# Performance work log

Measured on AMD Instinct MI355X. Metric: run time of the kernel, lower is better.

The kernel has to match this reference:

```python
import jax, jax.numpy as jnp
import numpy as np


def exp_segsum(x):
    """exp(segsum(x)) with the -inf mask folded into a zero mask (same math).
    x: (..., T) -> (..., T, T) lower-triangular decay matrix."""
    T = x.shape[-1]
    xr = jnp.broadcast_to(x[..., None], (*x.shape, T))  # (..., d, e) = x[..., d]
    lower = jnp.tril(jnp.ones((T, T), dtype=bool), -1)
    seg = jnp.cumsum(jnp.where(lower, xr, 0.0), axis=-2)
    incl = jnp.tril(jnp.ones((T, T), dtype=bool), 0)
    return jnp.where(incl, jnp.exp(seg), 0.0)


def ssd(x, A, B, C, chunk_size):
    """Mamba2 chunked structured state-space duality.
    x: (b, L, h, p); A: (b, L, h); B, C: (b, L, n) (shared across heads).
    Returns y: (b, L, h, p) and final state (b, h, p, n)."""
    b_, L_, H, P = x.shape
    c = L_ // chunk_size
    xm = x.reshape(b_, c, chunk_size, H, P)                      # b c l h p
    Am = A.reshape(b_, c, chunk_size, H).transpose(0, 3, 1, 2)   # b h c l
    Bm = B.reshape(b_, c, chunk_size, -1)                        # b c l n
    Cm = C.reshape(b_, c, chunk_size, -1)                        # b c l n
    A_cumsum = jnp.cumsum(Am, axis=-1)                           # b h c l
    Lmat = exp_segsum(Am)                                        # b h c l l
    # intra-chunk (diagonal block) outputs
    Y_diag = jnp.einsum('bcln,bcsn,bhcls,bcshp->bclhp', Cm, Bm, Lmat, xm)
    # per-chunk states
    decay_states = jnp.exp(A_cumsum[:, :, :, -1:] - A_cumsum)    # b h c l
    states = jnp.einsum('bcln,bhcl,bclhp->bchpn', Bm, decay_states, xm)
    init = jnp.zeros_like(states[:, :1])
    states = jnp.concatenate([init, states], axis=1)             # b (c+1) h p n
    # inter-chunk recurrence via segsum over chunk-level decays
    decay_chunk = exp_segsum(jnp.pad(A_cumsum[:, :, :, -1], ((0, 0), (0, 0), (1, 0))))
    new_states = jnp.einsum('bhzc,bchpn->bzhpn', decay_chunk, states)
    states, final_state = new_states[:, :-1], new_states[:, -1]
    # state -> output conversion
    decay_out = jnp.exp(A_cumsum)                                # b h c l
    Y_off = jnp.einsum('bcln,bchpn,bhcl->bclhp', Cm, states, decay_out)
    Y = (Y_diag + Y_off).reshape(b_, L_, H, P)
    return Y, final_state


def setup_inputs() -> dict:
    key = jax.random.key(0)
    ks = jax.random.split(key, 4)
    B, L, d_model = 2, 4096, 1024
    expand, head_dim, d_state, d_conv, chunk = 2, 64, 128, 4, 64
    d_inner = d_model * expand           # 2048
    n_heads = d_inner // head_dim        # 32
    d_in_proj = 2 * d_inner + 2 * d_state + n_heads  # 4384
    conv_dim = d_inner + 2 * d_state     # 2304
    x = jax.random.normal(ks[0], (B, L, d_model), jnp.float32)
    in_proj_w = jax.random.normal(ks[1], (d_model, d_in_proj), jnp.float32) / np.sqrt(d_model)
    conv_w = jax.random.normal(ks[2], (d_conv, 1, conv_dim), jnp.float32) * np.sqrt(2.0 / d_conv)
    conv_b = jnp.zeros((conv_dim,), jnp.float32)
    dt_bias = jnp.full((n_heads,), 0.1, jnp.float32)
    A_log = jnp.full((n_heads,), -1.0, jnp.float32)
    D = jnp.full((n_heads,), 0.1, jnp.float32)
    norm_scale = jnp.ones((d_inner,), jnp.float32)
    out_proj_w = jax.random.normal(ks[3], (d_inner, d_model), jnp.float32) / np.sqrt(d_inner)
    return {"x": x, "in_proj_w": in_proj_w, "conv_w": conv_w, "conv_b": conv_b,
            "dt_bias": dt_bias, "A_log": A_log, "D": D, "norm_scale": norm_scale,
            "out_proj_w": out_proj_w, "chunk_size": chunk}


def reference(x, in_proj_w, conv_w, conv_b, dt_bias, A_log, D, norm_scale, out_proj_w, chunk_size):
    n_heads = dt_bias.shape[0]
    d_inner = norm_scale.shape[0]
    head_dim = d_inner // n_heads
    conv_dim = conv_b.shape[0]
    d_state = (conv_dim - d_inner) // 2
    k = conv_w.shape[0]
    A = -jnp.exp(A_log)                                           # (H,)
    zxbcdt = x @ in_proj_w                                        # (B, L, d_in_proj)
    z = zxbcdt[..., :d_inner]
    xbc = zxbcdt[..., d_inner:d_inner + conv_dim]
    dt = jax.nn.softplus(zxbcdt[..., -n_heads:] + dt_bias)       # (B, L, H)
    # causal depthwise conv (pad k-1 both sides then take first L == pad (k-1, 0))
    xbc = jax.lax.conv_general_dilated(
        xbc, conv_w, window_strides=(1,), padding=[(k - 1, 0)],
        dimension_numbers=('NWC', 'WIO', 'NWC'), feature_group_count=conv_dim) + conv_b
    xbc = jax.nn.silu(xbc)
    xs = xbc[..., :d_inner]
    b = xbc[..., d_inner:d_inner + d_state]
    c = xbc[..., d_inner + d_state:]
    xs = xs.reshape(*xs.shape[:2], n_heads, head_dim)            # (B, L, H, P)
    y, ssm_state = ssd(xs * dt[..., None], A * dt, b, c, chunk_size)
    y = y + xs * D[..., None]
    y = y.reshape(*y.shape[:2], d_inner)
    # gated RMSNorm (Mamba2 norm(y, z))
    yz = y * jax.nn.silu(z)
    y = yz * jax.lax.rsqrt(jnp.mean(yz * yz, axis=-1, keepdims=True) + 1e-6) * norm_scale
    return y @ out_proj_w
```

## Files before the change

kernel.cpp:

```cpp
#include <hip/hip_runtime.h>
#include <hip/hip_bf16.h>
#include <math.h>

typedef __hip_bfloat16 bf16;
typedef __attribute__((ext_vector_type(8))) short short8;
typedef __attribute__((ext_vector_type(4))) float f32x4;

constexpr int BB    = 2;
constexpr int LL    = 4096;
constexpr int DM    = 1024;
constexpr int DIN   = 2048;
constexpr int HH    = 32;
constexpr int PP    = 64;
constexpr int NSD   = 128;
constexpr int CONVD = 2304;
constexpr int DPROJ = 4384;
constexpr int NPAD  = 4480;
constexpr int CHK   = 64;
constexpr int NC    = 64;
constexpr int ROWS  = BB * LL;

__device__ __forceinline__ float b2f(bf16 v) { return __bfloat162float(v); }
__device__ __forceinline__ bf16  f2b(float f) { return __float2bfloat16(f); }
__device__ __forceinline__ short f2bs(float f) {
  bf16 b = f2b(f);
  return *reinterpret_cast<short*>(&b);
}
__device__ __forceinline__ void gload16(const short* g, short* l) {
  __builtin_amdgcn_global_load_lds(
      (const __attribute__((address_space(1))) void*)g,
      (__attribute__((address_space(3))) void*)l, 16, 0, 0);
}

__global__ __launch_bounds__(256) void convert_bf16(const float* __restrict__ in,
                                                    bf16* __restrict__ outp, int n4) {
  int i = blockIdx.x * 256 + threadIdx.x;
  if (i >= n4) return;
  float4 v = *(const float4*)&in[(size_t)i * 4];
  bf16* p = &outp[(size_t)i * 4];
  p[0] = f2b(v.x); p[1] = f2b(v.y); p[2] = f2b(v.z); p[3] = f2b(v.w);
}

__global__ __launch_bounds__(256) void transpose_w(const float* __restrict__ W,
                                                   bf16* __restrict__ Bt,
                                                   int K, int N) {
  __shared__ float Tl[32][33];
  const int n0 = blockIdx.x * 32, k0 = blockIdx.y * 32;
  const int t = threadIdx.x;
  {
    const int kk = t >> 3, nn4 = (t & 7) * 4;
#pragma unroll
    for (int j = 0; j < 4; ++j) {
      int n = n0 + nn4 + j;
      Tl[kk][nn4 + j] = (n < N) ? W[(size_t)(k0 + kk) * N + n] : 0.f;
    }
  }
  __syncthreads();
  {
    const int nn = t >> 3, kk4 = (t & 7) * 4;
#pragma unroll
    for (int j = 0; j < 4; ++j)
      Bt[(size_t)(n0 + nn) * K + k0 + kk4 + j] = f2b(Tl[kk4 + j][nn]);
  }
}

template <int MODE>
__global__ __launch_bounds__(256) void gemm_mfma(
    const short* __restrict__ A, const short* __restrict__ Bt, int K,
    bf16* __restrict__ zb, bf16* __restrict__ xbcb,
    float* __restrict__ dtraw, float* __restrict__ Cout) {
  __shared__ short Asl[2][128 * 32];
  __shared__ short Bsl[2][128 * 32];
  const int t = threadIdx.x;
  const int l = t & 63;
  const int w = t >> 6;
  const int wr = w >> 1, wc = w & 1;
  const int m0 = blockIdx.y * 128;
  const int n0 = blockIdx.x * 128;

  const int srow = l >> 2;
  const int sk   = (((l & 3) - ((l >> 3) & 3)) & 3) * 8;
  const short* gA0 = &A [(size_t)(m0 + (w    ) * 16 + srow) * K + sk];
  const short* gA1 = &A [(size_t)(m0 + (4 + w) * 16 + srow) * K + sk];
  const short* gB0 = &Bt[(size_t)(n0 + (w    ) * 16 + srow) * K + sk];
  const short* gB1 = &Bt[(size_t)(n0 + (4 + w) * 16 + srow) * K + sk];
  const int ldsA0 = (w * 16) * 32, ldsA1 = ((4 + w) * 16) * 32;

  const int fr = l & 15;
  const int s2 = (((l >> 4) + ((fr >> 1) & 3)) & 3) * 8;
  const int aoff = (wr * 64 + fr) * 32 + s2;
  const int boff = (wc * 64 + fr) * 32 + s2;

  f32x4 acc[4][4] = {};
  const int nt = K >> 5;

  gload16(gA0, &Asl[0][ldsA0]); gload16(gA1, &Asl[0][ldsA1]);
  gload16(gB0, &Bsl[0][ldsA0]); gload16(gB1, &Bsl[0][ldsA1]);
  gA0 += 32; gA1 += 32; gB0 += 32; gB1 += 32;
  __syncthreads();

  for (int ti = 0; ti < nt; ++ti) {
    const int cur = ti & 1;
    if (ti + 1 < nt) {
      const int nxt = cur ^ 1;
      gload16(gA0, &Asl[nxt][ldsA0]); gload16(gA1, &Asl[nxt][ldsA1]);
      gload16(gB0, &Bsl[nxt][ldsA0]); gload16(gB1, &Bsl[nxt][ldsA1]);
      gA0 += 32; gA1 += 32; gB0 += 32; gB1 += 32;
    }
    short8 af[4], bg[4];
#pragma unroll
    for (int i = 0; i < 4; ++i) {
      af[i] = *(const short8*)&Asl[cur][aoff + i * 512];
      bg[i] = *(const short8*)&Bsl[cur][boff + i * 512];
    }
#pragma unroll
    for (int i = 0; i < 4; ++i)
#pragma unroll
      for (int j = 0; j < 4; ++j)
        acc[i][j] = __builtin_amdgcn_mfma_f32_16x16x32_bf16(af[i], bg[j],
                                                            acc[i][j], 0, 0, 0);
    __syncthreads();
  }
#pragma unroll
  for (int i = 0; i < 4; ++i) {
#pragma unroll
    for (int j = 0; j < 4; ++j) {
      int gcol = n0 + wc * 64 + j * 16 + (l & 15);
      int grow0 = m0 + wr * 64 + i * 16 + (l >> 4) * 4;
#pragma unroll
      for (int q = 0; q < 4; ++q) {
        float v = acc[i][j][q];
        int grow = grow0 + q;
        if constexpr (MODE == 0) {
          if (gcol < DIN) {
            zb[(size_t)grow * DIN + gcol] = f2b(v);
          } else if (gcol < DIN + CONVD) {
            xbcb[(size_t)grow * CONVD + (gcol - DIN)] = f2b(v);
          } else if (gcol < DPROJ) {
            dtraw[(size_t)grow * HH + (gcol - DIN - CONVD)] = v;
          }
        } else {
          Cout[(size_t)grow * DM + gcol] = v;
        }
      }
    }
  }
}

__global__ __launch_bounds__(256) void conv_act(
    const bf16* __restrict__ xbc, const float* __restrict__ dtraw,
    const float* __restrict__ convw, const float* __restrict__ convb,
    const float* __restrict__ dtb, const float* __restrict__ alog,
    bf16* __restrict__ xs, bf16* __restrict__ Bb, bf16* __restrict__ Cb,
    float* __restrict__ dtv, float* __restrict__ dtA) {
  const int row = blockIdx.x;
  const int l   = row & (LL - 1);
  const int t   = threadIdx.x;
  if (t < HH) {
    float raw = dtraw[(size_t)row * HH + t] + dtb[t];
    float dt  = (raw > 20.f) ? raw : log1pf(expf(raw));
    dtv[(size_t)row * HH + t] = dt;
    dtA[(size_t)row * HH + t] = -expf(alog[t]) * dt;
  }
  for (int ch = t * 8; ch < CONVD; ch += 2048) {
    float acc[8];
#pragma unroll
    for (int j = 0; j < 8; ++j) acc[j] = convb[ch + j];
#pragma unroll
    for (int k = 0; k < 4; ++k) {
      if (l - 3 + k >= 0) {
        uint4 v = *(const uint4*)&xbc[(size_t)(row - 3 + k) * CONVD + ch];
        const bf16* pv = (const bf16*)&v;
        const float* wp = &convw[k * CONVD + ch];
#pragma unroll
        for (int j = 0; j < 8; ++j) acc[j] += b2f(pv[j]) * wp[j];
      }
    }
    short8 sv;
#pragma unroll
    for (int j = 0; j < 8; ++j) {
      float s = acc[j] / (1.f + expf(-acc[j]));
      sv[j] = f2bs(s);
    }
    if (ch < DIN) {
      *(short8*)&xs[(size_t)row * DIN + ch] = sv;
    } else if (ch < DIN + NSD) {
      *(short8*)&Bb[(size_t)row * NSD + (ch - DIN)] = sv;
    } else {
      *(short8*)&Cb[(size_t)row * NSD + (ch - DIN - NSD)] = sv;
    }
  }
}

__global__ __launch_bounds__(256) void gmat(const bf16* __restrict__ Bb,
                                            const bf16* __restrict__ Cb,
                                            float* __restrict__ G) {
  const int c = blockIdx.x, b = blockIdx.y;
  const int row0 = (b * NC + c) * CHK;
  __shared__ short Csh[64][136];
  __shared__ short Bsh[64][136];
  const int t = threadIdx.x;
  const int lane = t & 63, w = t >> 6;
#pragma unroll
  for (int i = 0; i < 4; ++i) {
    int f = t + i * 256;
    int rr = f >> 4, n0 = (f & 15) * 8;
    *(uint4*)&Csh[rr][n0] = *(const uint4*)&Cb[(size_t)(row0 + rr) * NSD + n0];
    *(uint4*)&Bsh[rr][n0] = *(const uint4*)&Bb[(size_t)(row0 + rr) * NSD + n0];
  }
  __syncthreads();
  f32x4 acc[4] = {};
  const int r = lane & 15, hi = lane >> 4;
#pragma unroll
  for (int kk = 0; kk < 4; ++kk) {
    short8 af = *(const short8*)&Csh[16 * w + r][kk * 32 + hi * 8];
#pragma unroll
    for (int j = 0; j < 4; ++j) {
      short8 bg = *(const short8*)&Bsh[16 * j + r][kk * 32 + hi * 8];
      acc[j] = __builtin_amdgcn_mfma_f32_16x16x32_bf16(af, bg, acc[j], 0, 0, 0);
    }
  }
#pragma unroll
  for (int j = 0; j < 4; ++j)
#pragma unroll
    for (int q = 0; q < 4; ++q) {
      int ll = 16 * w + hi * 4 + q, ss = 16 * j + r;
      G[((size_t)(b * NC + c) * CHK + ll) * CHK + ss] = acc[j][q];
    }
}

__global__ __launch_bounds__(256) void ssd_chunk(
    const float* __restrict__ G, const bf16* __restrict__ xsp,
    const bf16* __restrict__ Bb, const float* __restrict__ dtv,
    const float* __restrict__ dtA,
    bf16* __restrict__ y, bf16* __restrict__ states, float* __restrict__ cumA) {
  const int h = blockIdx.x, c = blockIdx.y, b = blockIdx.z;
  const int row0 = (b * NC + c) * CHK;
  __shared__ short GMb[64][72];
  __shared__ short xdsT[64][72];
  __shared__ short BdT[128][72];
  __shared__ float sA[CHK], cA[CHK], dec[CHK], sdt[CHK];
  const int t = threadIdx.x;
  const int lane = t & 63, w = t >> 6;
  if (t < CHK) {
    sA[t]  = dtA[(size_t)(row0 + t) * HH + h];
    sdt[t] = dtv[(size_t)(row0 + t) * HH + h];
  }
  __syncthreads();
  if (t == 0) {
    float s = 0.f;
    for (int i = 0; i < CHK; ++i) { s += sA[i]; cA[i] = s; }
  }
  __syncthreads();
  if (t < CHK) {
    dec[t] = expf(cA[CHK - 1] - cA[t]);
    cumA[((size_t)(b * HH + h) * NC + c) * CHK + t] = cA[t];
  }
#pragma unroll
  for (int i = 0; i < 2; ++i) {
    int f = t + i * 256;
    int ll = f >> 3, p0 = (f & 7) * 8;
    uint4 v = *(const uint4*)&xsp[(size_t)(row0 + ll) * DIN + h * PP + p0];
    const bf16* pv = (const bf16*)&v;
    float dtl = sdt[ll];
#pragma unroll
    for (int j = 0; j < 8; ++j) xdsT[p0 + j][ll] = f2bs(b2f(pv[j]) * dtl);
  }
#pragma unroll
  for (int i = 0; i < 4; ++i) {
    int f = t + i * 256;
    int ll = f >> 4, s0 = (f & 15) * 4;
    float4 g = *(const float4*)&G[((size_t)(b * NC + c) * CHK + ll) * CHK + s0];
    float ca = cA[ll];
    GMb[ll][s0 + 0] = f2bs((s0 + 0 <= ll) ? g.x * expf(ca - cA[s0 + 0]) : 0.f);
    GMb[ll][s0 + 1] = f2bs((s0 + 1 <= ll) ? g.y * expf(ca - cA[s0 + 1]) : 0.f);
    GMb[ll][s0 + 2] = f2bs((s0 + 2 <= ll) ? g.z * expf(ca - cA[s0 + 2]) : 0.f);
    GMb[ll][s0 + 3] = f2bs((s0 + 3 <= ll) ? g.w * expf(ca - cA[s0 + 3]) : 0.f);
  }
  __syncthreads();
#pragma unroll
  for (int i = 0; i < 4; ++i) {
    int f = t + i * 256;
    int ll = f >> 4, n0 = (f & 15) * 8;
    uint4 v = *(const uint4*)&Bb[(size_t)(row0 + ll) * NSD + n0];
    const bf16* pv = (const bf16*)&v;
    float dl = dec[ll];
#pragma unroll
    for (int j = 0; j < 8; ++j) BdT[n0 + j][ll] = f2bs(b2f(pv[j]) * dl);
  }
  __syncthreads();
  const int r = lane & 15, hi = lane >> 4;
  {
    f32x4 acc[4] = {};
#pragma unroll
    for (int kk = 0; kk < 2; ++kk) {
      short8 af = *(const short8*)&GMb[16 * w + r][kk * 32 + hi * 8];
#pragma unroll
      for (int j = 0; j < 4; ++j) {
        short8 bg = *(const short8*)&xdsT[16 * j + r][kk * 32 + hi * 8];
        acc[j] = __builtin_amdgcn_mfma_f32_16x16x32_bf16(af, bg, acc[j], 0, 0, 0);
      }
    }
#pragma unroll
    for (int j = 0; j < 4; ++j)
#pragma unroll
      for (int q = 0; q < 4; ++q) {
        int ll = 16 * w + hi * 4 + q, pp = 16 * j + r;
        y[(size_t)(row0 + ll) * DIN + h * PP + pp] = f2b(acc[j][q]);
      }
  }
  {
    f32x4 acc[8] = {};
#pragma unroll
    for (int kk = 0; kk < 2; ++kk) {
      short8 af = *(const short8*)&xdsT[16 * w + r][kk * 32 + hi * 8];
#pragma unroll
      for (int j = 0; j < 8; ++j) {
        short8 bg = *(const short8*)&BdT[16 * j + r][kk * 32 + hi * 8];
        acc[j] = __builtin_amdgcn_mfma_f32_16x16x32_bf16(af, bg, acc[j], 0, 0, 0);
      }
    }
    size_t sb = ((size_t)(b * NC + c) * HH + h) * (PP * NSD);
#pragma unroll
    for (int j = 0; j < 8; ++j)
#pragma unroll
      for (int q = 0; q < 4; ++q) {
        int pp = 16 * w + hi * 4 + q, nn = 16 * j + r;
        states[sb + (size_t)pp * NSD + nn] = f2b(acc[j][q]);
      }
  }
}

__global__ __launch_bounds__(256) void scan(bf16* __restrict__ states,
                                            const float* __restrict__ cumA) {
  const int q = blockIdx.x, h = blockIdx.y, b = blockIdx.z;
  const int t = threadIdx.x;
  float S[8] = {};
  for (int c = 0; c < NC; ++c) {
    float tot = expf(cumA[((size_t)(b * HH + h) * NC + c) * CHK + CHK - 1]);
    size_t base = ((size_t)(b * NC + c) * HH + h) * (PP * NSD) + q * 2048 + t;
#pragma unroll
    for (int i = 0; i < 8; ++i) {
      float cs = b2f(states[base + i * 256]);
      states[base + i * 256] = f2b(S[i]);
      S[i] = S[i] * tot + cs;
    }
  }
}

__global__ __launch_bounds__(256) void yoff(
    const bf16* __restrict__ Cb, const bf16* __restrict__ states,
    const float* __restrict__ cumA, const bf16* __restrict__ xs,
    const float* __restrict__ Dp, bf16* __restrict__ y) {
  const int h = blockIdx.x, c = blockIdx.y, b = blockIdx.z;
  const int row0 = (b * NC + c) * CHK;
  __shared__ short Csh[64][136];
  __shared__ short Ssh[64][136];
  __shared__ float dcy[CHK];
  const int t = threadIdx.x;
  const int lane = t & 63, w = t >> 6;
  if (t < CHK) dcy[t] = expf(cumA[((size_t)(b * HH + h) * NC + c) * CHK + t]);
  const size_t sbase = ((size_t)(b * NC + c) * HH + h) * (PP * NSD);
#pragma unroll
  for (int i = 0; i < 4; ++i) {
    int f = t + i * 256;
    int rr = f >> 4, n0 = (f & 15) * 8;
    *(uint4*)&Csh[rr][n0] = *(const uint4*)&Cb[(size_t)(row0 + rr) * NSD + n0];
    *(uint4*)&Ssh[rr][n0] = *(const uint4*)&states[sbase + (size_t)rr * NSD + n0];
  }
  __syncthreads();
  f32x4 acc[4] = {};
  const int r = lane & 15, hi = lane >> 4;
#pragma unroll
  for (int kk = 0; kk < 4; ++kk) {
    short8 af = *(const short8*)&Csh[16 * w + r][kk * 32 + hi * 8];
#pragma unroll
    for (int j = 0; j < 4; ++j) {
      short8 bg = *(const short8*)&Ssh[16 * j + r][kk * 32 + hi * 8];
      acc[j] = __builtin_amdgcn_mfma_f32_16x16x32_bf16(af, bg, acc[j], 0, 0, 0);
    }
  }
  const float Dh = Dp[h];
#pragma unroll
  for (int j = 0; j < 4; ++j)
#pragma unroll
    for (int q = 0; q < 4; ++q) {
      int ll = 16 * w + hi * 4 + q, pp = 16 * j + r;
      size_t idx = (size_t)(row0 + ll) * DIN + h * PP + pp;
      y[idx] = f2b(b2f(y[idx]) + acc[j][q] * dcy[ll] + b2f(xs[idx]) * Dh);
    }
}

__global__ __launch_bounds__(256) void gatenorm(const bf16* __restrict__ y,
                                                const bf16* __restrict__ zb,
                                                const float* __restrict__ nsc,
                                                bf16* __restrict__ outn) {
  const int row = blockIdx.x, t = threadIdx.x;
  float v[8];
  float ss = 0.f;
#pragma unroll
  for (int i = 0; i < 8; ++i) {
    int ch = t + i * 256;
    float z  = b2f(zb[(size_t)row * DIN + ch]);
    float yv = b2f(y[(size_t)row * DIN + ch]);
    float g  = yv * z / (1.f + expf(-z));
    v[i] = g;
    ss += g * g;
  }
#pragma unroll
  for (int off = 32; off > 0; off >>= 1) ss += __shfl_down(ss, off, 64);
  __shared__ float red[4];
  if ((t & 63) == 0) red[t >> 6] = ss;
  __syncthreads();
  float tot = red[0] + red[1] + red[2] + red[3];
  float r = rsqrtf(tot * (1.f / DIN) + 1e-6f);
#pragma unroll
  for (int i = 0; i < 8; ++i) {
    int ch = t + i * 256;
    outn[(size_t)row * DIN + ch] = f2b(v[i] * r * nsc[ch]);
  }
}

extern "C" void kernel_launch(void* const* d_in, const int* in_sizes, int n_in,
                              void* d_out, int out_size, void* d_ws, size_t ws_size,
                              hipStream_t stream) {
  const float* x     = (const float*)d_in[0];
  const float* inw   = (const float*)d_in[1];
  const float* convw = (const float*)d_in[2];
  const float* convb = (const float*)d_in[3];
  const float* dtb   = (const float*)d_in[4];
  const float* alog  = (const float*)d_in[5];
  const float* Dp    = (const float*)d_in[6];
  const float* nsc   = (const float*)d_in[7];
  const float* outw  = (const float*)d_in[8];
  float* out = (float*)d_out;

  char* p = (char*)d_ws;
  bf16*  zb     = (bf16*)p;  p += (size_t)ROWS * DIN * 2;
  bf16*  xbcb   = (bf16*)p;  p += (size_t)ROWS * CONVD * 2;
  bf16*  y      = xbcb;
  float* dtraw  = (float*)p; p += (size_t)ROWS * HH * 4;
  bf16*  xs     = (bf16*)p;  p += (size_t)ROWS * DIN * 2;
  bf16*  states = (bf16*)p;  p += (size_t)BB * NC * HH * PP * NSD * 2;
  bf16*  normb  = states;
  bf16*  Bb     = (bf16*)p;  p += (size_t)ROWS * NSD * 2;
  bf16*  Cb     = (bf16*)p;  p += (size_t)ROWS * NSD * 2;
  float* dtv    = (float*)p; p += (size_t)ROWS * HH * 4;
  float* dtA    = (float*)p; p += (size_t)ROWS * HH * 4;
  float* cumA   = (float*)p; p += (size_t)BB * HH * NC * CHK * 4;
  float* G      = (float*)p; p += (size_t)BB * NC * CHK * CHK * 4;
  bf16*  xb     = (bf16*)p;  p += (size_t)ROWS * DM * 2;
  bf16*  BtIn   = (bf16*)p;  p += (size_t)NPAD * DM * 2;
  bf16*  BtOut  = xb;

  convert_bf16<<<(ROWS * DM / 4 + 255) / 256, 256, 0, stream>>>(x, xb, ROWS * DM / 4);
  transpose_w<<<dim3(NPAD / 32, DM / 32), 256, 0, stream>>>(inw, BtIn, DM, DPROJ);
  gemm_mfma<0><<<dim3(NPAD / 128, ROWS / 128), 256, 0, stream>>>(
      (const short*)xb, (const short*)BtIn, DM, zb, xbcb, dtraw, nullptr);
  transpose_w<<<dim3(DM / 32, DIN / 32), 256, 0, stream>>>(outw, BtOut, DIN, DM);
  conv_act<<<ROWS, 256, 0, stream>>>(xbcb, dtraw, convw, convb, dtb, alog,
                                     xs, Bb, Cb, dtv, dtA);
  gmat<<<dim3(NC, BB), 256, 0, stream>>>(Bb, Cb, G);
  ssd_chunk<<<dim3(HH, NC, BB), 256, 0, stream>>>(G, xs, Bb, dtv, dtA,
                                                  y, states, cumA);
  scan<<<dim3(4, HH, BB), 256, 0, stream>>>(states, cumA);
  yoff<<<dim3(HH, NC, BB), 256, 0, stream>>>(Cb, states, cumA, xs, Dp, y);
  gatenorm<<<ROWS, 256, 0, stream>>>(y, zb, nsc, normb);
  gemm_mfma<1><<<dim3(DM / 128, ROWS / 128), 256, 0, stream>>>(
      (const short*)normb, (const short*)BtOut, DIN, nullptr, nullptr, nullptr, out);

  (void)in_sizes; (void)n_in; (void)out_size; (void)ws_size;
}
```

Baseline: 354.7 us.

## Pipeline GEMM loads with vmcnt waits, shrink out-proj tile, vectorize scan and gatenorm

The GEMM now uses explicit vmcnt waits and raw barriers in place of __syncthreads, so the next tile's global-to-LDS loads stay in flight while the current tile is consumed. It also gains an MI template for a 64-row tile, used for the output projection to launch more blocks. The scan kernel switches to 16-byte vector loads and stores and prefetches the next chunk's states. Gatenorm uses vectorized 8-element loads and stores. The hand-written waitcnt values are fragile if the compiler reorders or adds memory ops.

```diff
diff --git a/kernel.cpp b/kernel.cpp
--- a/kernel.cpp
+++ b/kernel.cpp
@@ -31,6 +31,14 @@
       (const __attribute__((address_space(1))) void*)g,
       (__attribute__((address_space(3))) void*)l, 16, 0, 0);
 }
+template <int N> __device__ __forceinline__ void waitvm() {
+  if constexpr (N == 0)      asm volatile("s_waitcnt vmcnt(0)" ::: "memory");
+  else if constexpr (N == 3) asm volatile("s_waitcnt vmcnt(3)" ::: "memory");
+  else                       asm volatile("s_waitcnt vmcnt(4)" ::: "memory");
+}
+__device__ __forceinline__ void barrier_raw() {
+  asm volatile("s_barrier" ::: "memory");
+}
 
 __global__ __launch_bounds__(256) void convert_bf16(const float* __restrict__ in,
                                                     bf16* __restrict__ outp, int n4) {
@@ -64,69 +72,80 @@
   }
 }
 
-template <int MODE>
+template <int MODE, int MI>
 __global__ __launch_bounds__(256) void gemm_mfma(
     const short* __restrict__ A, const short* __restrict__ Bt, int K,
     bf16* __restrict__ zb, bf16* __restrict__ xbcb,
     float* __restrict__ dtraw, float* __restrict__ Cout) {
-  __shared__ short Asl[2][128 * 32];
+  constexpr int MROWS = MI * 32;
+  constexpr int NV = (MI == 4) ? 4 : 3;
+  __shared__ short Asl[2][MROWS * 32];
   __shared__ short Bsl[2][128 * 32];
   const int t = threadIdx.x;
   const int l = t & 63;
   const int w = t >> 6;
   const int wr = w >> 1, wc = w & 1;
-  const int m0 = blockIdx.y * 128;
+  const int m0 = blockIdx.y * MROWS;
   const int n0 = blockIdx.x * 128;
 
   const int srow = l >> 2;
   const int sk   = (((l & 3) - ((l >> 3) & 3)) & 3) * 8;
-  const short* gA0 = &A [(size_t)(m0 + (w    ) * 16 + srow) * K + sk];
-  const short* gA1 = &A [(size_t)(m0 + (4 + w) * 16 + srow) * K + sk];
-  const short* gB0 = &Bt[(size_t)(n0 + (w    ) * 16 + srow) * K + sk];
+  const short* gA0 = &A [(size_t)(m0 + w * 16 + srow) * K + sk];
+  const short* gA1 = (MI == 4) ? &A[(size_t)(m0 + (4 + w) * 16 + srow) * K + sk]
+                               : gA0;
+  const short* gB0 = &Bt[(size_t)(n0 + w * 16 + srow) * K + sk];
   const short* gB1 = &Bt[(size_t)(n0 + (4 + w) * 16 + srow) * K + sk];
-  const int ldsA0 = (w * 16) * 32, ldsA1 = ((4 + w) * 16) * 32;
+  const int ldsW0 = (w * 16) * 32, ldsW1 = ((4 + w) * 16) * 32;
+
+  auto STAGE = [&](int buf) {
+    gload16(gA0, &Asl[buf][ldsW0]);
+    if constexpr (MI == 4) gload16(gA1, &Asl[buf][ldsW1]);
+    gload16(gB0, &Bsl[buf][ldsW0]);
+    gload16(gB1, &Bsl[buf][ldsW1]);
+    gA0 += 32; if constexpr (MI == 4) gA1 += 32;
+    gB0 += 32; gB1 += 32;
+  };
 
   const int fr = l & 15;
   const int s2 = (((l >> 4) + ((fr >> 1) & 3)) & 3) * 8;
-  const int aoff = (wr * 64 + fr) * 32 + s2;
+  const int aoff = (wr * (MI * 16) + fr) * 32 + s2;
   const int boff = (wc * 64 + fr) * 32 + s2;
 
-  f32x4 acc[4][4] = {};
+  f32x4 acc[MI][4] = {};
   const int nt = K >> 5;
 
-  gload16(gA0, &Asl[0][ldsA0]); gload16(gA1, &Asl[0][ldsA1]);
-  gload16(gB0, &Bsl[0][ldsA0]); gload16(gB1, &Bsl[0][ldsA1]);
-  gA0 += 32; gA1 += 32; gB0 += 32; gB1 += 32;
-  __syncthreads();
+  STAGE(0);
+  waitvm<0>();
+  barrier_raw();
 
   for (int ti = 0; ti < nt; ++ti) {
     const int cur = ti & 1;
+    if (ti) barrier_raw();
     if (ti + 1 < nt) {
-      const int nxt = cur ^ 1;
-      gload16(gA0, &Asl[nxt][ldsA0]); gload16(gA1, &Asl[nxt][ldsA1]);
-      gload16(gB0, &Bsl[nxt][ldsA0]); gload16(gB1, &Bsl[nxt][ldsA1]);
-      gA0 += 32; gA1 += 32; gB0 += 32; gB1 += 32;
-    }
-    short8 af[4], bg[4];
-#pragma unroll
-    for (int i = 0; i < 4; ++i) {
-      af[i] = *(const short8*)&Asl[cur][aoff + i * 512];
-      bg[i] = *(const short8*)&Bsl[cur][boff + i * 512];
-    }
-#pragma unroll
-    for (int i = 0; i < 4; ++i)
+      STAGE(cur ^ 1);
+      waitvm<NV>();
+    } else {
+      waitvm<0>();
+    }
+    barrier_raw();
+    short8 af[MI], bg[4];
+#pragma unroll
+    for (int i = 0; i < MI; ++i) af[i] = *(const short8*)&Asl[cur][aoff + i * 512];
+#pragma unroll
+    for (int j = 0; j < 4; ++j)  bg[j] = *(const short8*)&Bsl[cur][boff + j * 512];
+#pragma unroll
+    for (int i = 0; i < MI; ++i)
 #pragma unroll
       for (int j = 0; j < 4; ++j)
         acc[i][j] = __builtin_amdgcn_mfma_f32_16x16x32_bf16(af[i], bg[j],
                                                             acc[i][j], 0, 0, 0);
-    __syncthreads();
-  }
-#pragma unroll
-  for (int i = 0; i < 4; ++i) {
+  }
+#pragma unroll
+  for (int i = 0; i < MI; ++i) {
 #pragma unroll
     for (int j = 0; j < 4; ++j) {
       int gcol = n0 + wc * 64 + j * 16 + (l & 15);
-      int grow0 = m0 + wr * 64 + i * 16 + (l >> 4) * 4;
+      int grow0 = m0 + wr * (MI * 16) + i * 16 + (l >> 4) * 4;
 #pragma unroll
       for (int q = 0; q < 4; ++q) {
         float v = acc[i][j][q];
@@ -335,16 +354,26 @@
                                             const float* __restrict__ cumA) {
   const int q = blockIdx.x, h = blockIdx.y, b = blockIdx.z;
   const int t = threadIdx.x;
+  const int off = q * 2048 + t * 8;
+  const size_t cstride = (size_t)HH * PP * NSD;
+  size_t base = ((size_t)(b * NC) * HH + h) * (PP * NSD) + off;
+  const float* cp = &cumA[(size_t)(b * HH + h) * NC * CHK + CHK - 1];
   float S[8] = {};
+  uint4 nv = *(const uint4*)&states[base];
   for (int c = 0; c < NC; ++c) {
-    float tot = expf(cumA[((size_t)(b * HH + h) * NC + c) * CHK + CHK - 1]);
-    size_t base = ((size_t)(b * NC + c) * HH + h) * (PP * NSD) + q * 2048 + t;
+    uint4 cv = nv;
+    if (c + 1 < NC) nv = *(const uint4*)&states[base + cstride];
+    float tot = expf(cp[(size_t)c * CHK]);
+    const bf16* pin = (const bf16*)&cv;
+    short8 sv;
 #pragma unroll
     for (int i = 0; i < 8; ++i) {
-      float cs = b2f(states[base + i * 256]);
-      states[base + i * 256] = f2b(S[i]);
+      float cs = b2f(pin[i]);
+      sv[i] = f2bs(S[i]);
       S[i] = S[i] * tot + cs;
     }
+    *(short8*)&states[base] = sv;
+    base += cstride;
   }
 }
 
@@ -396,14 +425,17 @@
                                                 const float* __restrict__ nsc,
                                                 bf16* __restrict__ outn) {
   const int row = blockIdx.x, t = threadIdx.x;
+  const int ch = t * 8;
+  uint4 yv4 = *(const uint4*)&y [(size_t)row * DIN + ch];
+  uint4 zv4 = *(const uint4*)&zb[(size_t)row * DIN + ch];
+  const bf16* yp = (const bf16*)&yv4;
+  const bf16* zp = (const bf16*)&zv4;
   float v[8];
   float ss = 0.f;
 #pragma unroll
   for (int i = 0; i < 8; ++i) {
-    int ch = t + i * 256;
-    float z  = b2f(zb[(size_t)row * DIN + ch]);
-    float yv = b2f(y[(size_t)row * DIN + ch]);
-    float g  = yv * z / (1.f + expf(-z));
+    float z  = b2f(zp[i]);
+    float g  = b2f(yp[i]) * z / (1.f + expf(-z));
     v[i] = g;
     ss += g * g;
   }
@@ -414,11 +446,10 @@
   __syncthreads();
   float tot = red[0] + red[1] + red[2] + red[3];
   float r = rsqrtf(tot * (1.f / DIN) + 1e-6f);
-#pragma unroll
-  for (int i = 0; i < 8; ++i) {
-    int ch = t + i * 256;
-    outn[(size_t)row * DIN + ch] = f2b(v[i] * r * nsc[ch]);
-  }
+  short8 o;
+#pragma unroll
+  for (int i = 0; i < 8; ++i) o[i] = f2bs(v[i] * r * nsc[ch + i]);
+  *(short8*)&outn[(size_t)row * DIN + ch] = o;
 }
 
 extern "C" void kernel_launch(void* const* d_in, const int* in_sizes, int n_in,
@@ -455,7 +486,7 @@
 
   convert_bf16<<<(ROWS * DM / 4 + 255) / 256, 256, 0, stream>>>(x, xb, ROWS * DM / 4);
   transpose_w<<<dim3(NPAD / 32, DM / 32), 256, 0, stream>>>(inw, BtIn, DM, DPROJ);
-  gemm_mfma<0><<<dim3(NPAD / 128, ROWS / 128), 256, 0, stream>>>(
+  gemm_mfma<0, 4><<<dim3(NPAD / 128, ROWS / 128), 256, 0, stream>>>(
       (const short*)xb, (const short*)BtIn, DM, zb, xbcb, dtraw, nullptr);
   transpose_w<<<dim3(DM / 32, DIN / 32), 256, 0, stream>>>(outw, BtOut, DIN, DM);
   conv_act<<<ROWS, 256, 0, stream>>>(xbcb, dtraw, convw, convb, dtb, alog,
@@ -466,7 +497,7 @@
   scan<<<dim3(4, HH, BB), 256, 0, stream>>>(states, cumA);
   yoff<<<dim3(HH, NC, BB), 256, 0, stream>>>(Cb, states, cumA, xs, Dp, y);
   gatenorm<<<ROWS, 256, 0, stream>>>(y, zb, nsc, normb);
-  gemm_mfma<1><<<dim3(DM / 128, ROWS / 128), 256, 0, stream>>>(
+  gemm_mfma<1, 2><<<dim3(DM / 128, ROWS / 64), 256, 0, stream>>>(
       (const short*)normb, (const short*)BtOut, DIN, nullptr, nullptr, nullptr, out);
 
   (void)in_sizes; (void)n_in; (void)out_size; (void)ws_size;
```

Measured after the change: 356.6 us. Within noise of the previous version (+0.5%).
